# Performance work log

Measured on AMD Instinct MI355X. Metric: run time of the kernel, lower is better.

Reference implementation:

```python
import jax, jax.numpy as jnp
import numpy as np

GRID = 16
PAD = 32
RADIUS = 8
SIGMA = 1.5
B = 8192
N_SEEDS = 24


def setup_inputs() -> dict:
    key = jax.random.key(0)
    k1, k2 = jax.random.split(key)
    # predicted seeds: (x, y, phase), coords in [0, GRID)
    output = jax.random.uniform(k1, (B, N_SEEDS * 3), dtype=jnp.float32) * GRID
    # target seeds: (x, y, amp), coords in [0, 2*GRID)
    targets = jax.random.uniform(k2, (B, N_SEEDS * 3), dtype=jnp.float32) * (2 * GRID)
    return {"output": output, "targets": targets}


def _forward(output, targets):
    Bn = output.shape[0]
    seeds = output.reshape(Bn, -1, 3)   # (B, N, 3): x, y, phase
    tgt = targets.reshape(Bn, -1, 3)    # (B, M, 3): x, y, amp

    # --- discrete Voronoi on GRID x GRID (vectorized over batch) ---
    c = jnp.arange(GRID, dtype=output.dtype)
    xx, yy = jnp.meshgrid(c, c, indexing='ij')  # (GRID, GRID)
    dist = jnp.sqrt((xx[None, :, :, None] - seeds[:, None, None, :, 0]) ** 2
                    + (yy[None, :, :, None] - seeds[:, None, None, :, 1]) ** 2)
    labels = jnp.argmin(dist, axis=-1)  # (B, GRID, GRID) int

    # circular support on the inner grid (np.ogrid[-r:r, -r:r] convention)
    cc = jnp.arange(-RADIUS, RADIUS)
    inner = (cc[:, None] ** 2 + cc[None, :] ** 2) <= RADIUS ** 2
    labels = jnp.where(inner[None], labels, 0)

    # zero-pad voronoi labels to PAD x PAD
    pw = (PAD - GRID) // 2
    padded = jnp.pad(labels, ((0, 0), (pw, pw), (pw, pw)))  # (B, PAD, PAD)

    # --- gather phase per pixel, zero outside circle on padded grid ---
    phases = seeds[:, :, 2]  # (B, N)
    phase = jnp.take_along_axis(phases, padded.reshape(Bn, -1), axis=1).reshape(Bn, PAD, PAD)
    pc = jnp.arange(PAD)
    center = PAD // 2
    outside = (pc[:, None] - center) ** 2 + (pc[None, :] - center) ** 2 > RADIUS ** 2
    phase = jnp.where(outside[None], jnp.zeros_like(phase), phase)

    # --- density = amp(=1) * exp(i * 2*pi * phase), shifted FFT magnitude ---
    two_pi = 2.0 * jnp.pi
    density = jax.lax.complex(jnp.cos(two_pi * phase), jnp.sin(two_pi * phase))
    pred = jnp.fft.fftshift(density, axes=(-2, -1))
    pred = jnp.fft.fft2(pred)
    pred_dp = jnp.abs(jnp.fft.fftshift(pred, axes=(-2, -1)))  # (B, PAD, PAD)

    # --- target diffraction: sum of Gaussians on (2*GRID)x(2*GRID) grid ---
    xc = jnp.arange(PAD, dtype=targets.dtype)  # height == width == 2*GRID == PAD
    tx = tgt[:, :, 0][:, :, None, None]
    ty = tgt[:, :, 1][:, :, None, None]
    amp = tgt[:, :, 2][:, :, None, None]
    # torch: x varies along last axis, y along second-to-last
    d2 = (xc[None, None, None, :] - tx) ** 2 + (xc[None, None, :, None] - ty) ** 2
    tgt_dp = jnp.sum(amp * jnp.exp(-d2 / (2.0 * SIGMA ** 2)), axis=1)  # (B, PAD, PAD)

    # --- chi-square (global max-normalization and reductions) ---
    p = pred_dp / jnp.max(pred_dp)
    t = tgt_dp / jnp.max(tgt_dp)
    return jnp.sum((p - t) ** 2) / jnp.sqrt(jnp.sum(p ** 2) * jnp.sum(t ** 2))


def reference(output, targets):
    return _forward(output, targets)
```

## Files before the change

kernel.cpp:

```cpp
#include <hip/hip_runtime.h>
#include <math.h>

#define NS 24

typedef float v2f __attribute__((ext_vector_type(2)));
typedef float v4f __attribute__((ext_vector_type(4)));


struct PixTab { unsigned short v[196]; };
__device__ constexpr PixTab make_pix() {
    PixTab t{};
    int n = 0;
    const int w[16] = {0,3,5,6,6,7,7,7,8,7,7,7,6,6,5,3};
    for (int yy = 0; yy < 16; ++yy)
        for (int x = 16 - w[yy]; x <= 16 + w[yy]; ++x)
            if (x < 24) { t.v[n] = (unsigned short)((yy << 8) | x); n = n + 1; }
    t.v[195] = (unsigned short)((8 << 8) | 24);
    return t;
}
__device__ constexpr PixTab PIX = make_pix();

struct ZTab { unsigned short v[76]; };
__device__ constexpr ZTab make_ztab() {
    ZTab z{};
    bool mark[16][17] = {};
    const int w[16] = {0,3,5,6,6,7,7,7,8,7,7,7,6,6,5,3};
    for (int yy = 0; yy < 16; ++yy)
        for (int x = 16 - w[yy]; x <= 16 + w[yy]; ++x)
            if (x < 24) mark[yy][x - 8] = true;
    mark[8][16] = true;
    int n = 0;
    for (int yy = 0; yy < 16; ++yy)
        for (int xi = 0; xi < 17; ++xi)
            if (!mark[yy][xi]) { z.v[n] = (unsigned short)(yy * 18 + xi); n = n + 1; }
    return z;
}
__device__ constexpr ZTab ZT = make_ztab();

constexpr float twc_(int p) {
    const float C[17] = {
        1.0f, 0.98078528040323044913f, 0.92387953251128675613f, 0.83146961230254523708f,
        0.70710678118654752440f, 0.55557023301960222474f, 0.38268343236508977173f,
        0.19509032201612826785f, 0.0f,
        -0.19509032201612826785f, -0.38268343236508977173f, -0.55557023301960222474f,
        -0.70710678118654752440f, -0.83146961230254523708f, -0.92387953251128675613f,
        -0.98078528040323044913f, -1.0f };
    return (p <= 16) ? C[p] : C[32 - p];
}
constexpr float tws_(int p) {
    const float S[17] = {
        0.0f, 0.19509032201612826785f, 0.38268343236508977173f, 0.55557023301960222474f,
        0.70710678118654752440f, 0.83146961230254523708f, 0.92387953251128675613f,
        0.98078528040323044913f, 1.0f,
        0.98078528040323044913f, 0.92387953251128675613f, 0.83146961230254523708f,
        0.70710678118654752440f, 0.55557023301960222474f, 0.38268343236508977173f,
        0.19509032201612826785f, 0.0f };
    return (p <= 16) ? -S[p] : S[32 - p];
}
struct alignas(16) TW1T { float v[8 * 18 * 2]; };
__device__ constexpr TW1T make_tw1() {
    TW1T t{};
    for (int l0 = 0; l0 < 8; ++l0)
        for (int xi = 0; xi < 17; ++xi) {
            int p = (l0 * (xi + 8)) & 31;
            t.v[(l0 * 18 + xi) * 2 + 0] = twc_(p);
            t.v[(l0 * 18 + xi) * 2 + 1] = tws_(p);
        }
    return t;
}
__device__ constexpr TW1T TW1G = make_tw1();
struct alignas(16) TW2T { float v[4 * 18 * 2]; };
__device__ constexpr TW2T make_tw2() {
    TW2T t{};
    for (int k0 = 0; k0 < 4; ++k0)
        for (int yp = 0; yp < 16; ++yp) {
            int p = (k0 * (yp + 8)) & 31;
            t.v[(k0 * 18 + yp) * 2 + 0] = twc_(p);
            t.v[(k0 * 18 + yp) * 2 + 1] = tws_(p);
        }
    return t;
}
__device__ constexpr TW2T TW2G = make_tw2();

static __device__ __forceinline__ v2f cmul(v2f e, v2f w) {
    v2f m = (v2f){e.y, e.y} * (v2f){w.y, w.x};
    return __builtin_elementwise_fma((v2f){e.x, e.x}, w, (v2f){-m.x, m.y});
}
static __device__ __forceinline__ float mag(v2f h) {
    v2f q = h * h;
    return sqrtf(q.x + q.y);
}

template <int CTRL>
static __device__ __forceinline__ float dpp_step(float x) {
    int y = __builtin_amdgcn_update_dpp(0, __float_as_int(x), CTRL, 0xf, 0xf, true);
    return __int_as_float(y);
}
static __device__ __forceinline__ float wave_sum(float x) {
    x += dpp_step<0x111>(x);
    x += dpp_step<0x112>(x);
    x += dpp_step<0x114>(x);
    x += dpp_step<0x118>(x);
    x += dpp_step<0x142>(x);
    x += dpp_step<0x143>(x);
    return x;
}
static __device__ __forceinline__ float wave_max(float x) {
    x = fmaxf(x, dpp_step<0x111>(x));
    x = fmaxf(x, dpp_step<0x112>(x));
    x = fmaxf(x, dpp_step<0x114>(x));
    x = fmaxf(x, dpp_step<0x118>(x));
    x = fmaxf(x, dpp_step<0x142>(x));
    x = fmaxf(x, dpp_step<0x143>(x));
    return x;
}

__global__ __launch_bounds__(256)
void loss_main(const float* __restrict__ output, const float* __restrict__ targets,
               float* __restrict__ partials, int B) {
    __shared__ float2 e24s;
    __shared__ __align__(16) float gx[NS * 32];
    __shared__ __align__(16) float gyT[32 * 24];
    __shared__ __align__(16) float e2f[16 * 18 * 2];
    __shared__ __align__(16) float tw1f[8 * 36];
    __shared__ __align__(16) float tw2f[4 * 36];
    __shared__ __align__(16) float gT2f[32 * 36];
    __shared__ __align__(16) float pmf[32 * 40];
    __shared__ float redm[2][5];

    const int b = blockIdx.x;
    const int t = threadIdx.x;
    const float* so = output + b * NS * 3;
    const float* tg = targets + b * NS * 3;

    if (t == 0) {
        float sv0, cv0;
        __sincosf(6.2831853071795864f * so[2], &sv0, &cv0);
        e24s = make_float2(cv0 - 1.0f, sv0);
    }
    if (t < 108) {
        if (t < 72) *(v4f*)&tw1f[t * 4] = *(const v4f*)&TW1G.v[t * 4];
        else        *(v4f*)&tw2f[(t - 72) * 4] = *(const v4f*)&TW2G.v[(t - 72) * 4];
    }
    for (int idx = t; idx < NS * 32; idx += 256) {
        int s = idx >> 5, c = idx & 31;
        float dx = (float)c - tg[3 * s];
        gx[idx] = tg[3 * s + 2] * __expf(dx * dx * (-1.0f / 4.5f));
    }
    for (int idx = t; idx < 32 * 24; idx += 256) {
        int r = idx / 24, s = idx - r * 24;
        float dy = (float)r - tg[3 * s + 1];
        gyT[idx] = __expf(dy * dy * (-1.0f / 4.5f));
    }
    if (t < 196) {
        int pv = PIX.v[t];
        int yy = pv >> 8, x = (pv & 255) - 8;
        float fi = (float)yy, fj = (float)x;
        float bd = 1e30f, bph = 0.f;
#pragma unroll
        for (int s = 0; s < NS; ++s) {
            float sx = so[3 * s], sy = so[3 * s + 1], phs = so[3 * s + 2];
            float dX = fi - sx;
            float dY = fj - sy;
            float d2 = __builtin_fmaf(dX, dX, dY * dY);
            if (d2 < bd) { bd = d2; bph = phs; }
        }
        float ph = (t == 195) ? so[2] : bph;
        float sv0, cv0;
        __sincosf(6.2831853071795864f * ph, &sv0, &cv0);
        *(v2f*)&e2f[(yy * 18 + x) * 2] = (v2f){cv0 - 1.0f, sv0};
    } else {
        int idx0 = t - 196;
        *(v2f*)&e2f[(int)ZT.v[idx0] * 2] = (v2f){0.f, 0.f};
        if (idx0 < 16)
            *(v2f*)&e2f[(int)ZT.v[idx0 + 60] * 2] = (v2f){0.f, 0.f};
    }
    __syncthreads();

    v2f ta01 = {0,0}, ta23 = {0,0}, tb01 = {0,0}, tb23 = {0,0};

    if (t < 128) {
        {
            int l0 = t >> 4, yy = t & 15;
            const float* row = &e2f[yy * 36];
            const float* twr = &tw1f[l0 * 36];
            v2f c0 = {0,0}, c1 = {0,0}, c2 = {0,0}, c3 = {0,0};
#pragma unroll
            for (int q = 0; q < 8; ++q) {
                v4f e4 = *(const v4f*)&row[q * 4];
                v4f w4 = *(const v4f*)&twr[q * 4];
                v2f ca = cmul((v2f){e4.x, e4.y}, (v2f){w4.x, w4.y});
                v2f cb = cmul((v2f){e4.z, e4.w}, (v2f){w4.z, w4.w});
                if ((q & 1) == 0) { c0 += ca; c1 += cb; }
                else              { c2 += ca; c3 += cb; }
            }
            {
                v2f e16 = *(const v2f*)&row[32];
                v2f w16 = *(const v2f*)&twr[32];
                c0 += cmul(e16, w16);
            }
            v2f a = c0 + c2, bb = c0 - c2;
            v2f cc = c1 + c3, d = c1 - c3;
            v2f du = {d.y, -d.x};
            *(v2f*)&gT2f[l0 * 36 + yy * 2]        = a + cc;
            *(v2f*)&gT2f[(l0 + 8) * 36 + yy * 2]  = bb + du;
            *(v2f*)&gT2f[(l0 + 16) * 36 + yy * 2] = a - cc;
            *(v2f*)&gT2f[(l0 + 24) * 36 + yy * 2] = bb - du;
        }
        __builtin_amdgcn_wave_barrier();

        {
            int base = (t >= 64) ? 4 : 0;
            int idx = t & 63;
            int lsel = idx >> 2;
            int l = base + (lsel & 3) + 8 * (lsel >> 2);
            int k0 = idx & 3;
            const float* gTr = &gT2f[l * 36];
            const float* twr = &tw2f[k0 * 36];
            v2f c[8];
#pragma unroll
            for (int q = 0; q < 4; ++q) {
                v4f glo = *(const v4f*)&gTr[q * 4];
                v4f ghi = *(const v4f*)&gTr[q * 4 + 16];
                v4f wlo = *(const v4f*)&twr[q * 4];
                v4f whi = *(const v4f*)&twr[q * 4 + 16];
                c[2 * q]     = cmul((v2f){glo.x, glo.y}, (v2f){wlo.x, wlo.y})
                             + cmul((v2f){ghi.x, ghi.y}, (v2f){whi.x, whi.y});
                c[2 * q + 1] = cmul((v2f){glo.z, glo.w}, (v2f){wlo.z, wlo.w})
                             + cmul((v2f){ghi.z, ghi.w}, (v2f){whi.z, whi.w});
            }
            v2f Ea = c[0] + c[4], Eb = c[0] - c[4];
            v2f Ec = c[2] + c[6], Ed = c[2] - c[6];
            v2f Edu = {Ed.y, -Ed.x};
            v2f E0 = Ea + Ec, E1 = Eb + Edu, E2 = Ea - Ec, E3 = Eb - Edu;
            v2f Oa = c[1] + c[5], Ob = c[1] - c[5];
            v2f Oc = c[3] + c[7], Od = c[3] - c[7];
            v2f Odu = {Od.y, -Od.x};
            v2f O0 = Oa + Oc, O1 = Ob + Odu, O2 = Oa - Oc, O3 = Ob - Odu;
            const float s2 = 0.70710678118654752440f;
            v2f w1O = (v2f){s2, s2} * (v2f){O1.x + O1.y, O1.y - O1.x};
            v2f w3O = (v2f){s2, s2} * (v2f){O3.y - O3.x, -(O3.x + O3.y)};
            v2f miO = {O2.y, -O2.x};
            {
                float2 e24 = e24s;
                float ar2 = (k0 == 0) ? 1.f : (k0 == 2) ? -1.f : 0.f;
                float ai2 = (k0 == 1) ? 1.f : (k0 == 3) ? -1.f : 0.f;
                float sgn = (l & 1) ? -1.f : 1.f;
                v2f T = {sgn * (e24.x * ar2 - e24.y * ai2),
                         sgn * (e24.x * ai2 + e24.y * ar2)};
                E0 += T; E1 += T; E2 += T; E3 += T;
            }
            v2f h0 = E0 + O0;
            if ((l | k0) == 0) h0.x += 1024.0f;
            int v = (l + 16) & 31;
            pmf[(k0 + 16) * 40 + v] = mag(h0);
            pmf[(k0 + 20) * 40 + v] = mag(E1 + w1O);
            pmf[(k0 + 24) * 40 + v] = mag(E2 + miO);
            pmf[(k0 + 28) * 40 + v] = mag(E3 + w3O);
            pmf[(k0)      * 40 + v] = mag(E0 - O0);
            pmf[(k0 + 4)  * 40 + v] = mag(E1 - w1O);
            pmf[(k0 + 8)  * 40 + v] = mag(E2 - miO);
            pmf[(k0 + 12) * 40 + v] = mag(E3 - w3O);
        }
    } else {
        int tid2 = t - 128;
        int r = tid2 >> 3;
        int c0i = (tid2 & 7) * 4;
#pragma unroll
        for (int q = 0; q < 6; ++q) {
            v4f gy4a = *(const v4f*)&gyT[r * 24 + q * 4];
            v4f gy4b = *(const v4f*)&gyT[(r + 16) * 24 + q * 4];
#pragma unroll
            for (int j = 0; j < 4; ++j) {
                v4f g4 = *(const v4f*)&gx[(4 * q + j) * 32 + c0i];
                float ga = (j == 0) ? gy4a.x : (j == 1) ? gy4a.y : (j == 2) ? gy4a.z : gy4a.w;
                float gb = (j == 0) ? gy4b.x : (j == 1) ? gy4b.y : (j == 2) ? gy4b.z : gy4b.w;
                v2f glo = {g4.x, g4.y}, ghi = {g4.z, g4.w};
                ta01 = __builtin_elementwise_fma((v2f){ga, ga}, glo, ta01);
                ta23 = __builtin_elementwise_fma((v2f){ga, ga}, ghi, ta23);
                tb01 = __builtin_elementwise_fma((v2f){gb, gb}, glo, tb01);
                tb23 = __builtin_elementwise_fma((v2f){gb, gb}, ghi, tb23);
            }
        }
    }
    __syncthreads();

    if (t >= 128) {
        int tid2 = t - 128;
        int r = tid2 >> 3;
        int c0i = (tid2 & 7) * 4;
        v4f p4a = *(const v4f*)&pmf[r * 40 + c0i];
        v4f p4b = *(const v4f*)&pmf[(r + 16) * 40 + c0i];
        v2f pa01 = {p4a.x, p4a.y}, pa23 = {p4a.z, p4a.w};
        v2f pb01 = {p4b.x, p4b.y}, pb23 = {p4b.z, p4b.w};
        v2f s2v = pa01 * pa01 + pa23 * pa23 + pb01 * pb01 + pb23 * pb23;
        v2f t2v = ta01 * ta01 + ta23 * ta23 + tb01 * tb01 + tb23 * tb23;
        v2f ptv = pa01 * ta01 + pa23 * ta23 + pb01 * tb01 + pb23 * tb23;
        float sp2 = s2v.x + s2v.y;
        float st2 = t2v.x + t2v.y;
        float spt = ptv.x + ptv.y;
        float mp = fmaxf(fmaxf(fmaxf(p4a.x, p4a.y), fmaxf(p4a.z, p4a.w)),
                         fmaxf(fmaxf(p4b.x, p4b.y), fmaxf(p4b.z, p4b.w)));
        v2f tm = __builtin_elementwise_max(__builtin_elementwise_max(ta01, ta23),
                                           __builtin_elementwise_max(tb01, tb23));
        float mt = fmaxf(tm.x, tm.y);
        sp2 = wave_sum(sp2);
        st2 = wave_sum(st2);
        spt = wave_sum(spt);
        mp  = wave_max(mp);
        mt  = wave_max(mt);
        int wv = (t >> 6) - 2, lane = t & 63;
        if (lane == 63) {
            redm[wv][0] = sp2; redm[wv][1] = st2; redm[wv][2] = spt;
            redm[wv][3] = mp;  redm[wv][4] = mt;
        }
    }
    __syncthreads();
    if (t == 0) {
        partials[0 * B + b] = redm[0][0] + redm[1][0];
        partials[1 * B + b] = redm[0][1] + redm[1][1];
        partials[2 * B + b] = redm[0][2] + redm[1][2];
        partials[3 * B + b] = fmaxf(redm[0][3], redm[1][3]);
        partials[4 * B + b] = fmaxf(redm[0][4], redm[1][4]);
    }
}

__global__ __launch_bounds__(1024)
void finalize_loss(const float* __restrict__ partials, float* __restrict__ out, int B) {
    __shared__ double reds[16][3];
    __shared__ float redx[16][2];
    const int t = threadIdx.x;
    double sp2 = 0.0, st2 = 0.0, spt = 0.0;
    float mp = 0.f, mt = 0.f;
    for (int i = t; i < B; i += 1024) {
        sp2 += (double)partials[0 * B + i];
        st2 += (double)partials[1 * B + i];
        spt += (double)partials[2 * B + i];
        mp = fmaxf(mp, partials[3 * B + i]);
        mt = fmaxf(mt, partials[4 * B + i]);
    }
    for (int off = 32; off > 0; off >>= 1) {
        sp2 += __shfl_down(sp2, off);
        st2 += __shfl_down(st2, off);
        spt += __shfl_down(spt, off);
        mp = fmaxf(mp, __shfl_down(mp, off));
        mt = fmaxf(mt, __shfl_down(mt, off));
    }
    int wave = t >> 6, lane = t & 63;
    if (lane == 0) {
        reds[wave][0] = sp2; reds[wave][1] = st2; reds[wave][2] = spt;
        redx[wave][0] = mp;  redx[wave][1] = mt;
    }
    __syncthreads();
    if (t == 0) {
        for (int w = 1; w < 16; ++w) {
            sp2 += reds[w][0];
            st2 += reds[w][1];
            spt += reds[w][2];
            mp = fmaxf(mp, redx[w][0]);
            mt = fmaxf(mt, redx[w][1]);
        }
        double Mp = (double)mp, Mt = (double)mt;
        double loss = (sp2 * (Mt / Mp) + st2 * (Mp / Mt) - 2.0 * spt) / sqrt(sp2 * st2);
        out[0] = (float)loss;
    }
}

extern "C" void kernel_launch(void* const* d_in, const int* in_sizes, int n_in,
                              void* d_out, int out_size, void* d_ws, size_t ws_size,
                              hipStream_t stream) {
    const float* output  = (const float*)d_in[0];
    const float* targets = (const float*)d_in[1];
    int B = in_sizes[0] / (NS * 3);
    float* partials = (float*)d_ws;

    loss_main<<<B, 256, 0, stream>>>(output, targets, partials, B);
    finalize_loss<<<1, 1024, 0, stream>>>(partials, (float*)d_out, B);
}
```

Baseline: 94.62 us.

## Fuse final reduction into main kernel via two-level atomic last-block election

Removes the separate finalize kernel launch. Each block writes its partial sums to an interleaved per-block record, then increments one of 64 padded group counters. The last block of each group bumps a global counter, and the final block overall performs the reduction and writes the loss. This trades the second launch for a memset launch, atomics and threadfences, and the final reduction now runs on only 256 threads.

```diff
diff --git a/kernel.cpp b/kernel.cpp
--- a/kernel.cpp
+++ b/kernel.cpp
@@ -117,7 +117,8 @@
 
 __global__ __launch_bounds__(256)
 void loss_main(const float* __restrict__ output, const float* __restrict__ targets,
-               float* __restrict__ partials, int B) {
+               float* __restrict__ partials, int* __restrict__ ctrs,
+               float* __restrict__ out, int B) {
     __shared__ float2 e24s;
     __shared__ __align__(16) float gx[NS * 32];
     __shared__ __align__(16) float gyT[32 * 24];
@@ -127,6 +128,9 @@
     __shared__ __align__(16) float gT2f[32 * 36];
     __shared__ __align__(16) float pmf[32 * 40];
     __shared__ float redm[2][5];
+    __shared__ double redd[4][3];
+    __shared__ float redf[4][2];
+    __shared__ int lastFlag;
 
     const int b = blockIdx.x;
     const int t = threadIdx.x;
@@ -317,52 +321,66 @@
     }
     __syncthreads();
     if (t == 0) {
-        partials[0 * B + b] = redm[0][0] + redm[1][0];
-        partials[1 * B + b] = redm[0][1] + redm[1][1];
-        partials[2 * B + b] = redm[0][2] + redm[1][2];
-        partials[3 * B + b] = fmaxf(redm[0][3], redm[1][3]);
-        partials[4 * B + b] = fmaxf(redm[0][4], redm[1][4]);
-    }
-}
-
-__global__ __launch_bounds__(1024)
-void finalize_loss(const float* __restrict__ partials, float* __restrict__ out, int B) {
-    __shared__ double reds[16][3];
-    __shared__ float redx[16][2];
-    const int t = threadIdx.x;
-    double sp2 = 0.0, st2 = 0.0, spt = 0.0;
-    float mp = 0.f, mt = 0.f;
-    for (int i = t; i < B; i += 1024) {
-        sp2 += (double)partials[0 * B + i];
-        st2 += (double)partials[1 * B + i];
-        spt += (double)partials[2 * B + i];
-        mp = fmaxf(mp, partials[3 * B + i]);
-        mt = fmaxf(mt, partials[4 * B + i]);
-    }
-    for (int off = 32; off > 0; off >>= 1) {
-        sp2 += __shfl_down(sp2, off);
-        st2 += __shfl_down(st2, off);
-        spt += __shfl_down(spt, off);
-        mp = fmaxf(mp, __shfl_down(mp, off));
-        mt = fmaxf(mt, __shfl_down(mt, off));
-    }
-    int wave = t >> 6, lane = t & 63;
-    if (lane == 0) {
-        reds[wave][0] = sp2; reds[wave][1] = st2; reds[wave][2] = spt;
-        redx[wave][0] = mp;  redx[wave][1] = mt;
+        v4f pv = {redm[0][0] + redm[1][0],
+                  redm[0][1] + redm[1][1],
+                  redm[0][2] + redm[1][2],
+                  fmaxf(redm[0][3], redm[1][3])};
+        *(v4f*)&partials[b * 8] = pv;
+        partials[b * 8 + 4] = fmaxf(redm[0][4], redm[1][4]);
+        __threadfence();
+        int g = b & 63;
+        int expect1 = (B >> 6) + (((B & 63) > g) ? 1 : 0);
+        int tk = atomicAdd(&ctrs[g << 6], 1);
+        int win = 0;
+        if (tk == expect1 - 1) {
+            __threadfence();
+            int ngroups = (B < 64) ? B : 64;
+            int tk2 = atomicAdd(&ctrs[64 * 64], 1);
+            win = (tk2 == ngroups - 1);
+        }
+        lastFlag = win;
     }
     __syncthreads();
-    if (t == 0) {
-        for (int w = 1; w < 16; ++w) {
-            sp2 += reds[w][0];
-            st2 += reds[w][1];
-            spt += reds[w][2];
-            mp = fmaxf(mp, redx[w][0]);
-            mt = fmaxf(mt, redx[w][1]);
-        }
-        double Mp = (double)mp, Mt = (double)mt;
-        double loss = (sp2 * (Mt / Mp) + st2 * (Mp / Mt) - 2.0 * spt) / sqrt(sp2 * st2);
-        out[0] = (float)loss;
+    if (!lastFlag) return;
+
+    __threadfence();
+    {
+        double sp2 = 0.0, st2 = 0.0, spt = 0.0;
+        float mp = 0.f, mt = 0.f;
+        for (int i = t; i < B; i += 256) {
+            v4f p = *(const v4f*)&partials[i * 8];
+            float m5 = partials[i * 8 + 4];
+            sp2 += (double)p.x;
+            st2 += (double)p.y;
+            spt += (double)p.z;
+            mp = fmaxf(mp, p.w);
+            mt = fmaxf(mt, m5);
+        }
+        for (int off = 32; off > 0; off >>= 1) {
+            sp2 += __shfl_down(sp2, off);
+            st2 += __shfl_down(st2, off);
+            spt += __shfl_down(spt, off);
+            mp = fmaxf(mp, __shfl_down(mp, off));
+            mt = fmaxf(mt, __shfl_down(mt, off));
+        }
+        int wv = t >> 6, lane = t & 63;
+        if (lane == 0) {
+            redd[wv][0] = sp2; redd[wv][1] = st2; redd[wv][2] = spt;
+            redf[wv][0] = mp;  redf[wv][1] = mt;
+        }
+        __syncthreads();
+        if (t == 0) {
+            for (int w2 = 1; w2 < 4; ++w2) {
+                sp2 += redd[w2][0];
+                st2 += redd[w2][1];
+                spt += redd[w2][2];
+                mp = fmaxf(mp, redf[w2][0]);
+                mt = fmaxf(mt, redf[w2][1]);
+            }
+            double Mp = (double)mp, Mt = (double)mt;
+            double loss = (sp2 * (Mt / Mp) + st2 * (Mp / Mt) - 2.0 * spt) / sqrt(sp2 * st2);
+            out[0] = (float)loss;
+        }
     }
 }
 
@@ -373,7 +391,9 @@
     const float* targets = (const float*)d_in[1];
     int B = in_sizes[0] / (NS * 3);
     float* partials = (float*)d_ws;
-
-    loss_main<<<B, 256, 0, stream>>>(output, targets, partials, B);
-    finalize_loss<<<1, 1024, 0, stream>>>(partials, (float*)d_out, B);
-}
+    int* ctrs = (int*)((char*)d_ws + (size_t)B * 8 * sizeof(float));
+
+    hipMemsetAsync(ctrs, 0, (64 * 64 + 64) * sizeof(int), stream);
+    loss_main<<<B, 256, 0, stream>>>(output, targets, partials, ctrs,
+                                     (float*)d_out, B);
+}
```

Result: slower. 215.1 us (+127.3%).
